# Kernel tuning notes

Hardware: AMD Instinct MI355X
Metric: run time of the kernel (lower is better)

The kernel has to match this reference:

```python
import jax, jax.numpy as jnp
import numpy as np

DIM = 256
NUM_HEADS = 8
WINDOW = 8


def setup_inputs() -> dict:
    key = jax.random.key(0)
    k1, k2, k3 = jax.random.split(key, 3)
    x = jax.random.normal(k1, (4, DIM, 256, 256), dtype=jnp.float32)
    w_qkv = jax.random.normal(k2, (3 * DIM, DIM), dtype=jnp.float32) * 0.02
    w_proj = jax.random.normal(k3, (DIM, DIM), dtype=jnp.float32) * 0.02
    return {"x": x, "w_qkv": w_qkv, "w_proj": w_proj}


def reference(x, w_qkv, w_proj):
    B, C, H, W = x.shape
    ws = WINDOW
    nh = NUM_HEADS
    hd = C // nh
    scale = float(hd) ** -0.5

    pad_h = (ws - H % ws) % ws
    pad_w = (ws - W % ws) % ws
    if pad_h or pad_w:
        x = jnp.pad(x, ((0, 0), (0, 0), (0, pad_h), (0, pad_w)))
    Hp, Wp = H + pad_h, W + pad_w
    nHw, nWw = Hp // ws, Wp // ws
    N = ws * ws

    # 1x1 conv QKV projection (no bias): [3C,C] x [B,C,Hp,Wp]
    qkv = jnp.einsum('oc,bchw->bohw', w_qkv, x)
    q, k, v = jnp.split(qkv, 3, axis=1)

    def partition(t):
        # [B,C,Hp,Wp] -> [B*nHw*nWw, nh, N, hd]
        t = t.reshape(B, nh, hd, nHw, ws, nWw, ws)
        t = t.transpose(0, 3, 5, 1, 4, 6, 2)  # B,nHw,nWw,nh,ws,ws,hd
        return t.reshape(B * nHw * nWw, nh, N, hd)

    qw = partition(q)
    kw = partition(k)
    vw = partition(v)

    attn = jnp.einsum('whnd,whmd->whnm', qw, kw) * scale
    attn = jax.nn.softmax(attn, axis=-1)
    out = jnp.einsum('whnm,whmd->whnd', attn, vw)  # [Bn, nh, N, hd]

    # unpartition: [Bn,nh,N,hd] -> [B,C,Hp,Wp]
    out = out.reshape(B, nHw, nWw, nh, ws, ws, hd)
    out = out.transpose(0, 3, 6, 1, 4, 2, 5)  # B,nh,hd,nHw,ws,nWw,ws
    out = out.reshape(B, C, Hp, Wp)

    out = jnp.einsum('oc,bchw->bohw', w_proj, out)
    if pad_h:
        out = out[:, :, :H, :]
    if pad_w:
        out = out[:, :, :, :W]
    return out
```

## Files before the change

kernel.cpp:

```cpp
#include <hip/hip_runtime.h>


#define DIMC 256
#define NH   8
#define HD   32
#define WS   8
#define NTOK 64
#define HRES 256
#define IMG  (HRES * HRES)

typedef _Float16 f16x8 __attribute__((ext_vector_type(8)));
typedef _Float16 f16x4 __attribute__((ext_vector_type(4)));
typedef float    f32x4 __attribute__((ext_vector_type(4)));

#define MFMA(a, b, c) __builtin_amdgcn_mfma_f32_16x16x32_f16((a), (b), (c), 0, 0, 0)

__global__ __launch_bounds__(256) void cvt_weights(const float* __restrict__ wqkv,
                                                   const float* __restrict__ wproj,
                                                   _Float16* __restrict__ wq,
                                                   _Float16* __restrict__ wp)
{
    int i = blockIdx.x * 256 + threadIdx.x;
    const int NQ = 768 * 256;
    const int NT = NQ + 256 * 256;
    if (i < NQ)      wq[i] = (_Float16)wqkv[i];
    else if (i < NT) wp[i - NQ] = (_Float16)wproj[i - NQ];
}

template <int PRE>
__device__ __forceinline__ f16x8 ldw(const void* w, int idx)
{
    if constexpr (PRE) {
        return *(const f16x8*)((const _Float16*)w + idx);
    } else {
        const float* p = (const float*)w + idx;
        f16x8 r;
        #pragma unroll
        for (int j = 0; j < 8; ++j) r[j] = (_Float16)p[j];
        return r;
    }
}

template <int PRE>
__global__ __launch_bounds__(512, 4)
void win_attn_mfma(const float* __restrict__ x,
                   const void* __restrict__ wqkv,
                   const void* __restrict__ wproj,
                   float* __restrict__ out)
{
    __shared__ _Float16 x_t[NTOK][DIMC + 8];
    __shared__ _Float16 q_t[NTOK][HD + 8];
    __shared__ _Float16 k_t[NTOK][HD + 8];
    __shared__ _Float16 v_c[HD][NTOK + 8];
    __shared__ _Float16 p_t[NTOK][NTOK + 8];
    __shared__ _Float16 ao_t[NTOK][HD + 8];

    const int t  = threadIdx.x;
    const int ln = t & 15;
    const int lq = (t & 63) >> 4;
    const int gu = __builtin_amdgcn_readfirstlane(t >> 6);
    const int b  = blockIdx.z;
    const int y0 = blockIdx.y * WS;
    const int x0 = blockIdx.x * WS;

    {
        const float* xb = x + (long)b * DIMC * IMG + (long)y0 * HRES + x0;
        #pragma unroll
        for (int i = 0; i < 4; ++i) {
            int qq = i * 512 + t;
            int c = qq >> 3, py = qq & 7;
            const float* src = xb + (long)c * IMG + py * HRES;
            float4 f0 = *(const float4*)src;
            float4 f1 = *(const float4*)(src + 4);
            int n = py * 8;
            x_t[n + 0][c] = (_Float16)f0.x; x_t[n + 1][c] = (_Float16)f0.y;
            x_t[n + 2][c] = (_Float16)f0.z; x_t[n + 3][c] = (_Float16)f0.w;
            x_t[n + 4][c] = (_Float16)f1.x; x_t[n + 5][c] = (_Float16)f1.y;
            x_t[n + 6][c] = (_Float16)f1.z; x_t[n + 7][c] = (_Float16)f1.w;
        }
    }

    const f32x4 zero = {0.f, 0.f, 0.f, 0.f};
    f32x4 facc[8];
    #pragma unroll
    for (int i = 0; i < 8; ++i) facc[i] = zero;

    const float scale = 0.17677669529663687f;
    const int nt = gu & 3;
    const int og = (gu >> 2) * 3;
    const int nrow = nt * 16 + ln;

    auto qkv_head = [&](int h) {
        f32x4 a0c = zero, a1c = zero, a2c = zero;
        const int wr0 = (((og + 0) >> 1) * DIMC + h * HD + (((og + 0) & 1) << 4) + ln) * DIMC;
        const int wr1 = (((og + 1) >> 1) * DIMC + h * HD + (((og + 1) & 1) << 4) + ln) * DIMC;
        const int wr2 = (((og + 2) >> 1) * DIMC + h * HD + (((og + 2) & 1) << 4) + ln) * DIMC;
        #pragma unroll
        for (int c0 = 0; c0 < DIMC; c0 += 32) {
            const int co = c0 + 8 * lq;
            f16x8 bx = *(const f16x8*)&x_t[nrow][co];
            f16x8 a0 = ldw<PRE>(wqkv, wr0 + co);
            f16x8 a1 = ldw<PRE>(wqkv, wr1 + co);
            f16x8 a2 = ldw<PRE>(wqkv, wr2 + co);
            a0c = MFMA(a0, bx, a0c);
            a1c = MFMA(a1, bx, a1c);
            a2c = MFMA(a2, bx, a2c);
        }
        #pragma unroll
        for (int j = 0; j < 3; ++j) {
            f32x4 a = (j == 0) ? a0c : ((j == 1) ? a1c : a2c);
            const int ot = og + j;
            const int part = ot >> 1;
            const int dbase = ((ot & 1) << 4) + 4 * lq;
            #pragma unroll
            for (int r = 0; r < 4; ++r) {
                const float v = a[r];
                const int d = dbase + r;
                if (part == 0)      q_t[nrow][d] = (_Float16)(v * scale);
                else if (part == 1) k_t[nrow][d] = (_Float16)v;
                else                v_c[d][nrow]  = (_Float16)v;
            }
        }
    };

    auto attn_head = [&]() {
        if (gu < 4) {
            const int qn = gu * 16 + ln;
            const int d8 = 8 * lq;
            f16x8 qf = *(const f16x8*)&q_t[qn][d8];
            f16x8 kf0 = *(const f16x8*)&k_t[ 0 + ln][d8];
            f16x8 kf1 = *(const f16x8*)&k_t[16 + ln][d8];
            f16x8 kf2 = *(const f16x8*)&k_t[32 + ln][d8];
            f16x8 kf3 = *(const f16x8*)&k_t[48 + ln][d8];
            f32x4 s0 = MFMA(kf0, qf, zero);
            f32x4 s1 = MFMA(kf1, qf, zero);
            f32x4 s2 = MFMA(kf2, qf, zero);
            f32x4 s3 = MFMA(kf3, qf, zero);
            float mx = -1e30f;
            #pragma unroll
            for (int r = 0; r < 4; ++r)
                mx = fmaxf(mx, fmaxf(fmaxf(s0[r], s1[r]), fmaxf(s2[r], s3[r])));
            mx = fmaxf(mx, __shfl_xor(mx, 16));
            mx = fmaxf(mx, __shfl_xor(mx, 32));
            float sum = 0.f;
            #pragma unroll
            for (int r = 0; r < 4; ++r) {
                s0[r] = __expf(s0[r] - mx); sum += s0[r];
                s1[r] = __expf(s1[r] - mx); sum += s1[r];
                s2[r] = __expf(s2[r] - mx); sum += s2[r];
                s3[r] = __expf(s3[r] - mx); sum += s3[r];
            }
            sum += __shfl_xor(sum, 16);
            sum += __shfl_xor(sum, 32);
            const float inv = 1.f / sum;
            const int kb = 4 * lq;
            f16x4 pv;
            #pragma unroll
            for (int r = 0; r < 4; ++r) pv[r] = (_Float16)(s0[r] * inv);
            *(f16x4*)&p_t[qn][ 0 + kb] = pv;
            #pragma unroll
            for (int r = 0; r < 4; ++r) pv[r] = (_Float16)(s1[r] * inv);
            *(f16x4*)&p_t[qn][16 + kb] = pv;
            #pragma unroll
            for (int r = 0; r < 4; ++r) pv[r] = (_Float16)(s2[r] * inv);
            *(f16x4*)&p_t[qn][32 + kb] = pv;
            #pragma unroll
            for (int r = 0; r < 4; ++r) pv[r] = (_Float16)(s3[r] * inv);
            *(f16x4*)&p_t[qn][48 + kb] = pv;

            f32x4 o0 = zero, o1 = zero;
            #pragma unroll
            for (int ks = 0; ks < 2; ++ks) {
                const int m0 = ks * 32 + 8 * lq;
                f16x8 pf = *(const f16x8*)&p_t[qn][m0];
                f16x8 v0 = *(const f16x8*)&v_c[ 0 + ln][m0];
                f16x8 v1 = *(const f16x8*)&v_c[16 + ln][m0];
                o0 = MFMA(v0, pf, o0);
                o1 = MFMA(v1, pf, o1);
            }
            const int db = 4 * lq;
            f16x4 av;
            #pragma unroll
            for (int r = 0; r < 4; ++r) av[r] = (_Float16)o0[r];
            *(f16x4*)&ao_t[qn][db] = av;
            #pragma unroll
            for (int r = 0; r < 4; ++r) av[r] = (_Float16)o1[r];
            *(f16x4*)&ao_t[qn][16 + db] = av;
        }
    };

    auto proj_head = [&](int h) {
        const int cb = h * HD + 8 * lq;
        f16x8 a0 = ldw<PRE>(wproj, ((gu * 2 + 0) * 16 + ln) * DIMC + cb);
        f16x8 a1 = ldw<PRE>(wproj, ((gu * 2 + 1) * 16 + ln) * DIMC + cb);
        #pragma unroll
        for (int np = 0; np < 4; ++np) {
            f16x8 bv = *(const f16x8*)&ao_t[np * 16 + ln][8 * lq];
            facc[np]     = MFMA(a0, bv, facc[np]);
            facc[4 + np] = MFMA(a1, bv, facc[4 + np]);
        }
    };

    __syncthreads();
    qkv_head(0);
    __syncthreads();
    for (int h = 0; h < NH; ++h) {
        attn_head();
        __syncthreads();
        proj_head(h);
        if (h < NH - 1) qkv_head(h + 1);
        __syncthreads();
    }

    {
        float* ob = out + (long)b * DIMC * IMG + (long)y0 * HRES + x0;
        #pragma unroll
        for (int i = 0; i < 8; ++i) {
            const int ot = gu * 2 + (i >> 2);
            const int n  = (i & 3) * 16 + ln;
            const int py = n >> 3, pxx = n & 7;
            float* op = ob + (long)(ot * 16 + 4 * lq) * IMG + py * HRES + pxx;
            op[0 * IMG] = facc[i][0];
            op[1 * IMG] = facc[i][1];
            op[2 * IMG] = facc[i][2];
            op[3 * IMG] = facc[i][3];
        }
    }
}

extern "C" void kernel_launch(void* const* d_in, const int* in_sizes, int n_in,
                              void* d_out, int out_size, void* d_ws, size_t ws_size,
                              hipStream_t stream)
{
    const float* x      = (const float*)d_in[0];
    const float* w_qkv  = (const float*)d_in[1];
    const float* w_proj = (const float*)d_in[2];
    float* out          = (float*)d_out;

    dim3 grid(HRES / WS, HRES / WS, 4);
    dim3 block(512);

    const size_t need = (size_t)(768 * 256 + 256 * 256) * sizeof(_Float16);
    if (d_ws && ws_size >= need) {
        _Float16* wq = (_Float16*)d_ws;
        _Float16* wp = wq + 768 * 256;
        hipLaunchKernelGGL(cvt_weights, dim3(1024), dim3(256), 0, stream,
                           w_qkv, w_proj, wq, wp);
        hipLaunchKernelGGL((win_attn_mfma<1>), grid, block, 0, stream,
                           x, (const void*)wq, (const void*)wp, out);
    } else {
        hipLaunchKernelGGL((win_attn_mfma<0>), grid, block, 0, stream,
                           x, (const void*)w_qkv, (const void*)w_proj, out);
    }
}
```

Measured before the change: 1.266 ms.

## Assign one head per wave and keep QKV/attention fragments in registers

The per-head loop with eight block-wide barriers is replaced by one head per wavefront. Q, K, V and P are kept in registers and rearranged into MFMA operand layout with lane shuffles instead of shared memory. The input tile is transposed with xor-shuffles so it can be written to shared memory as vectors, the full attention output is staged once before a single projection GEMM, and block indices are swizzled to change which windows run together. The cost is more registers and shuffle instructions per wave, which may lower occupancy.

```diff
diff --git a/kernel.cpp b/kernel.cpp
--- a/kernel.cpp
+++ b/kernel.cpp
@@ -9,6 +9,8 @@
 #define HRES 256
 #define IMG  (HRES * HRES)
 
+#define XPITCH 272
+
 typedef _Float16 f16x8 __attribute__((ext_vector_type(8)));
 typedef _Float16 f16x4 __attribute__((ext_vector_type(4)));
 typedef float    f32x4 __attribute__((ext_vector_type(4)));
@@ -39,6 +41,37 @@
         for (int j = 0; j < 8; ++j) r[j] = (_Float16)p[j];
         return r;
     }
+}
+
+__device__ __forceinline__ int2 shfl2(int2 v, int s)
+{
+    v.x = __shfl(v.x, s);
+    v.y = __shfl(v.y, s);
+    return v;
+}
+
+__device__ __forceinline__ int2 pack4(f32x4 a)
+{
+    f16x4 h;
+    h[0] = (_Float16)a[0]; h[1] = (_Float16)a[1];
+    h[2] = (_Float16)a[2]; h[3] = (_Float16)a[3];
+    return __builtin_bit_cast(int2, h);
+}
+
+__device__ __forceinline__ f16x8 cat8(int2 lo, int2 hi)
+{
+    int4 w = {lo.x, lo.y, hi.x, hi.y};
+    return __builtin_bit_cast(f16x8, w);
+}
+
+__device__ __forceinline__ f16x8 bfrag(int2 pu0, int2 pu1, int ln, int lq)
+{
+    const int slo = ln + 32 * (lq & 1);
+    int2 l0 = shfl2(pu0, slo), h0 = shfl2(pu0, slo + 16);
+    int2 l1 = shfl2(pu1, slo), h1 = shfl2(pu1, slo + 16);
+    int2 lo = (lq & 2) ? l1 : l0;
+    int2 hi = (lq & 2) ? h1 : h0;
+    return cat8(lo, hi);
 }
 
 template <int PRE>
@@ -48,183 +81,196 @@
                    const void* __restrict__ wproj,
                    float* __restrict__ out)
 {
-    __shared__ _Float16 x_t[NTOK][DIMC + 8];
-    __shared__ _Float16 q_t[NTOK][HD + 8];
-    __shared__ _Float16 k_t[NTOK][HD + 8];
-    __shared__ _Float16 v_c[HD][NTOK + 8];
-    __shared__ _Float16 p_t[NTOK][NTOK + 8];
-    __shared__ _Float16 ao_t[NTOK][HD + 8];
+    __shared__ _Float16 x_t[NTOK][XPITCH];
+    __shared__ _Float16 ao_t[NTOK][XPITCH];
 
     const int t  = threadIdx.x;
     const int ln = t & 15;
     const int lq = (t & 63) >> 4;
     const int gu = __builtin_amdgcn_readfirstlane(t >> 6);
-    const int b  = blockIdx.z;
-    const int y0 = blockIdx.y * WS;
-    const int x0 = blockIdx.x * WS;
+
+    const int lin = blockIdx.x + (blockIdx.y << 5) + (blockIdx.z << 10);
+    const int w   = ((lin & 7) << 9) | (lin >> 3);
+    const int b   = w >> 10;
+    const int y0  = ((w >> 5) & 31) * WS;
+    const int x0  = (w & 31) * WS;
+
+    const f32x4 zero = {0.f, 0.f, 0.f, 0.f};
+    const float scale = 0.17677669529663687f;
 
     {
-        const float* xb = x + (long)b * DIMC * IMG + (long)y0 * HRES + x0;
+        const int py = t & 7;
+        const int cg = (t & 63) >> 3;
+        const float* xb = x + (long)b * DIMC * IMG + (long)(y0 + py) * HRES + x0;
         #pragma unroll
         for (int i = 0; i < 4; ++i) {
-            int qq = i * 512 + t;
-            int c = qq >> 3, py = qq & 7;
-            const float* src = xb + (long)c * IMG + py * HRES;
+            const int cbase = i * 64 + gu * 8;
+            const float* src = xb + (long)(cbase + cg) * IMG;
             float4 f0 = *(const float4*)src;
             float4 f1 = *(const float4*)(src + 4);
-            int n = py * 8;
-            x_t[n + 0][c] = (_Float16)f0.x; x_t[n + 1][c] = (_Float16)f0.y;
-            x_t[n + 2][c] = (_Float16)f0.z; x_t[n + 3][c] = (_Float16)f0.w;
-            x_t[n + 4][c] = (_Float16)f1.x; x_t[n + 5][c] = (_Float16)f1.y;
-            x_t[n + 6][c] = (_Float16)f1.z; x_t[n + 7][c] = (_Float16)f1.w;
-        }
-    }
-
-    const f32x4 zero = {0.f, 0.f, 0.f, 0.f};
-    f32x4 facc[8];
+            float v[8] = {f0.x, f0.y, f0.z, f0.w, f1.x, f1.y, f1.z, f1.w};
+            #pragma unroll
+            for (int s = 1; s < 8; s <<= 1) {
+                float nv[8];
+                #pragma unroll
+                for (int j = 0; j < 8; ++j) {
+                    float ex = __shfl_xor(v[j ^ s], 8 * s);
+                    nv[j] = ((j ^ cg) & s) ? ex : v[j];
+                }
+                #pragma unroll
+                for (int j = 0; j < 8; ++j) v[j] = nv[j];
+            }
+            f16x8 hv;
+            #pragma unroll
+            for (int j = 0; j < 8; ++j) hv[j] = (_Float16)v[j];
+            *(f16x8*)&x_t[8 * py + cg][cbase] = hv;
+        }
+    }
+    __syncthreads();
+
+    int2 Qp[2][4], Kp[2][4], Vp[4][2];
     #pragma unroll
-    for (int i = 0; i < 8; ++i) facc[i] = zero;
-
-    const float scale = 0.17677669529663687f;
-    const int nt = gu & 3;
-    const int og = (gu >> 2) * 3;
-    const int nrow = nt * 16 + ln;
-
-    auto qkv_head = [&](int h) {
-        f32x4 a0c = zero, a1c = zero, a2c = zero;
-        const int wr0 = (((og + 0) >> 1) * DIMC + h * HD + (((og + 0) & 1) << 4) + ln) * DIMC;
-        const int wr1 = (((og + 1) >> 1) * DIMC + h * HD + (((og + 1) & 1) << 4) + ln) * DIMC;
-        const int wr2 = (((og + 2) >> 1) * DIMC + h * HD + (((og + 2) & 1) << 4) + ln) * DIMC;
-        #pragma unroll
-        for (int c0 = 0; c0 < DIMC; c0 += 32) {
-            const int co = c0 + 8 * lq;
-            f16x8 bx = *(const f16x8*)&x_t[nrow][co];
-            f16x8 a0 = ldw<PRE>(wqkv, wr0 + co);
-            f16x8 a1 = ldw<PRE>(wqkv, wr1 + co);
-            f16x8 a2 = ldw<PRE>(wqkv, wr2 + co);
-            a0c = MFMA(a0, bx, a0c);
-            a1c = MFMA(a1, bx, a1c);
-            a2c = MFMA(a2, bx, a2c);
-        }
-        #pragma unroll
-        for (int j = 0; j < 3; ++j) {
-            f32x4 a = (j == 0) ? a0c : ((j == 1) ? a1c : a2c);
-            const int ot = og + j;
-            const int part = ot >> 1;
-            const int dbase = ((ot & 1) << 4) + 4 * lq;
-            #pragma unroll
-            for (int r = 0; r < 4; ++r) {
-                const float v = a[r];
-                const int d = dbase + r;
-                if (part == 0)      q_t[nrow][d] = (_Float16)(v * scale);
-                else if (part == 1) k_t[nrow][d] = (_Float16)v;
-                else                v_c[d][nrow]  = (_Float16)v;
-            }
-        }
-    };
-
-    auto attn_head = [&]() {
-        if (gu < 4) {
-            const int qn = gu * 16 + ln;
-            const int d8 = 8 * lq;
-            f16x8 qf = *(const f16x8*)&q_t[qn][d8];
-            f16x8 kf0 = *(const f16x8*)&k_t[ 0 + ln][d8];
-            f16x8 kf1 = *(const f16x8*)&k_t[16 + ln][d8];
-            f16x8 kf2 = *(const f16x8*)&k_t[32 + ln][d8];
-            f16x8 kf3 = *(const f16x8*)&k_t[48 + ln][d8];
-            f32x4 s0 = MFMA(kf0, qf, zero);
-            f32x4 s1 = MFMA(kf1, qf, zero);
-            f32x4 s2 = MFMA(kf2, qf, zero);
-            f32x4 s3 = MFMA(kf3, qf, zero);
-            float mx = -1e30f;
-            #pragma unroll
-            for (int r = 0; r < 4; ++r)
-                mx = fmaxf(mx, fmaxf(fmaxf(s0[r], s1[r]), fmaxf(s2[r], s3[r])));
-            mx = fmaxf(mx, __shfl_xor(mx, 16));
-            mx = fmaxf(mx, __shfl_xor(mx, 32));
+    for (int mt = 0; mt < 2; ++mt) {
+        f32x4 aq[4], ak[4], av[4];
+        #pragma unroll
+        for (int nt = 0; nt < 4; ++nt) { aq[nt] = zero; ak[nt] = zero; av[nt] = zero; }
+        const int rq = (          gu * HD + 16 * mt + ln) * DIMC;
+        const int rk = (DIMC    + gu * HD + 16 * mt + ln) * DIMC;
+        const int rv = (2 * DIMC + gu * HD + 16 * mt + ln) * DIMC;
+        #pragma unroll
+        for (int ks = 0; ks < 8; ++ks) {
+            const int co = 32 * ks + 8 * lq;
+            f16x8 wqf = ldw<PRE>(wqkv, rq + co);
+            f16x8 wkf = ldw<PRE>(wqkv, rk + co);
+            f16x8 wvf = ldw<PRE>(wqkv, rv + co);
+            #pragma unroll
+            for (int nt = 0; nt < 4; ++nt) {
+                f16x8 xf = *(const f16x8*)&x_t[16 * nt + ln][co];
+                aq[nt] = MFMA(wqf, xf, aq[nt]);
+                ak[nt] = MFMA(wkf, xf, ak[nt]);
+                av[nt] = MFMA(xf, wvf, av[nt]);
+            }
+        }
+        #pragma unroll
+        for (int nt = 0; nt < 4; ++nt) {
+            Qp[mt][nt] = pack4(aq[nt] * scale);
+            Kp[mt][nt] = pack4(ak[nt]);
+            Vp[nt][mt] = pack4(av[nt]);
+        }
+    }
+
+    {
+        f16x8 kf[4], qf[4];
+        #pragma unroll
+        for (int kt = 0; kt < 4; ++kt) kf[kt] = bfrag(Kp[0][kt], Kp[1][kt], ln, lq);
+        #pragma unroll
+        for (int qt = 0; qt < 4; ++qt) qf[qt] = bfrag(Qp[0][qt], Qp[1][qt], ln, lq);
+
+        f32x4 s[4][4];
+        #pragma unroll
+        for (int kt = 0; kt < 4; ++kt)
+            #pragma unroll
+            for (int qt = 0; qt < 4; ++qt)
+                s[kt][qt] = MFMA(kf[kt], qf[qt], zero);
+
+        float inv[4];
+        #pragma unroll
+        for (int qt = 0; qt < 4; ++qt) {
+            float m = -1e30f;
+            #pragma unroll
+            for (int kt = 0; kt < 4; ++kt)
+                #pragma unroll
+                for (int r = 0; r < 4; ++r) m = fmaxf(m, s[kt][qt][r]);
+            m = fmaxf(m, __shfl_xor(m, 16));
+            m = fmaxf(m, __shfl_xor(m, 32));
             float sum = 0.f;
             #pragma unroll
-            for (int r = 0; r < 4; ++r) {
-                s0[r] = __expf(s0[r] - mx); sum += s0[r];
-                s1[r] = __expf(s1[r] - mx); sum += s1[r];
-                s2[r] = __expf(s2[r] - mx); sum += s2[r];
-                s3[r] = __expf(s3[r] - mx); sum += s3[r];
-            }
+            for (int kt = 0; kt < 4; ++kt)
+                #pragma unroll
+                for (int r = 0; r < 4; ++r) {
+                    float e = __expf(s[kt][qt][r] - m);
+                    s[kt][qt][r] = e;
+                    sum += e;
+                }
             sum += __shfl_xor(sum, 16);
             sum += __shfl_xor(sum, 32);
-            const float inv = 1.f / sum;
-            const int kb = 4 * lq;
-            f16x4 pv;
-            #pragma unroll
-            for (int r = 0; r < 4; ++r) pv[r] = (_Float16)(s0[r] * inv);
-            *(f16x4*)&p_t[qn][ 0 + kb] = pv;
-            #pragma unroll
-            for (int r = 0; r < 4; ++r) pv[r] = (_Float16)(s1[r] * inv);
-            *(f16x4*)&p_t[qn][16 + kb] = pv;
-            #pragma unroll
-            for (int r = 0; r < 4; ++r) pv[r] = (_Float16)(s2[r] * inv);
-            *(f16x4*)&p_t[qn][32 + kb] = pv;
-            #pragma unroll
-            for (int r = 0; r < 4; ++r) pv[r] = (_Float16)(s3[r] * inv);
-            *(f16x4*)&p_t[qn][48 + kb] = pv;
-
-            f32x4 o0 = zero, o1 = zero;
-            #pragma unroll
-            for (int ks = 0; ks < 2; ++ks) {
-                const int m0 = ks * 32 + 8 * lq;
-                f16x8 pf = *(const f16x8*)&p_t[qn][m0];
-                f16x8 v0 = *(const f16x8*)&v_c[ 0 + ln][m0];
-                f16x8 v1 = *(const f16x8*)&v_c[16 + ln][m0];
-                o0 = MFMA(v0, pf, o0);
-                o1 = MFMA(v1, pf, o1);
-            }
-            const int db = 4 * lq;
-            f16x4 av;
-            #pragma unroll
-            for (int r = 0; r < 4; ++r) av[r] = (_Float16)o0[r];
-            *(f16x4*)&ao_t[qn][db] = av;
-            #pragma unroll
-            for (int r = 0; r < 4; ++r) av[r] = (_Float16)o1[r];
-            *(f16x4*)&ao_t[qn][16 + db] = av;
-        }
-    };
-
-    auto proj_head = [&](int h) {
-        const int cb = h * HD + 8 * lq;
-        f16x8 a0 = ldw<PRE>(wproj, ((gu * 2 + 0) * 16 + ln) * DIMC + cb);
-        f16x8 a1 = ldw<PRE>(wproj, ((gu * 2 + 1) * 16 + ln) * DIMC + cb);
-        #pragma unroll
-        for (int np = 0; np < 4; ++np) {
-            f16x8 bv = *(const f16x8*)&ao_t[np * 16 + ln][8 * lq];
-            facc[np]     = MFMA(a0, bv, facc[np]);
-            facc[4 + np] = MFMA(a1, bv, facc[4 + np]);
-        }
-    };
-
+            inv[qt] = 1.f / sum;
+        }
+
+        int2 Pp[4][4];
+        #pragma unroll
+        for (int kt = 0; kt < 4; ++kt)
+            #pragma unroll
+            for (int qt = 0; qt < 4; ++qt)
+                Pp[kt][qt] = pack4(s[kt][qt] * inv[qt]);
+
+        f32x4 pv[2][4];
+        #pragma unroll
+        for (int dt = 0; dt < 2; ++dt)
+            #pragma unroll
+            for (int qt = 0; qt < 4; ++qt) pv[dt][qt] = zero;
+        #pragma unroll
+        for (int ks = 0; ks < 2; ++ks) {
+            f16x8 vf[2], pf[4];
+            #pragma unroll
+            for (int dt = 0; dt < 2; ++dt)
+                vf[dt] = bfrag(Vp[2 * ks][dt], Vp[2 * ks + 1][dt], ln, lq);
+            #pragma unroll
+            for (int qt = 0; qt < 4; ++qt)
+                pf[qt] = bfrag(Pp[2 * ks][qt], Pp[2 * ks + 1][qt], ln, lq);
+            #pragma unroll
+            for (int dt = 0; dt < 2; ++dt)
+                #pragma unroll
+                for (int qt = 0; qt < 4; ++qt)
+                    pv[dt][qt] = MFMA(vf[dt], pf[qt], pv[dt][qt]);
+        }
+
+        #pragma unroll
+        for (int dt = 0; dt < 2; ++dt)
+            #pragma unroll
+            for (int qt = 0; qt < 4; ++qt) {
+                f16x4 hv;
+                #pragma unroll
+                for (int r = 0; r < 4; ++r) hv[r] = (_Float16)pv[dt][qt][r];
+                *(f16x4*)&ao_t[16 * qt + ln][gu * HD + 16 * dt + 4 * lq] = hv;
+            }
+    }
     __syncthreads();
-    qkv_head(0);
-    __syncthreads();
-    for (int h = 0; h < NH; ++h) {
-        attn_head();
-        __syncthreads();
-        proj_head(h);
-        if (h < NH - 1) qkv_head(h + 1);
-        __syncthreads();
+
+    f32x4 fa[2][4];
+    #pragma unroll
+    for (int o = 0; o < 2; ++o)
+        #pragma unroll
+        for (int nt = 0; nt < 4; ++nt) fa[o][nt] = zero;
+    {
+        const int r0 = (16 * (2 * gu + 0) + ln) * DIMC;
+        const int r1 = (16 * (2 * gu + 1) + ln) * DIMC;
+        #pragma unroll
+        for (int ks = 0; ks < 8; ++ks) {
+            const int co = 32 * ks + 8 * lq;
+            f16x8 w0 = ldw<PRE>(wproj, r0 + co);
+            f16x8 w1 = ldw<PRE>(wproj, r1 + co);
+            #pragma unroll
+            for (int nt = 0; nt < 4; ++nt) {
+                f16x8 af = *(const f16x8*)&ao_t[16 * nt + ln][co];
+                fa[0][nt] = MFMA(w0, af, fa[0][nt]);
+                fa[1][nt] = MFMA(w1, af, fa[1][nt]);
+            }
+        }
     }
 
     {
         float* ob = out + (long)b * DIMC * IMG + (long)y0 * HRES + x0;
         #pragma unroll
-        for (int i = 0; i < 8; ++i) {
-            const int ot = gu * 2 + (i >> 2);
-            const int n  = (i & 3) * 16 + ln;
-            const int py = n >> 3, pxx = n & 7;
-            float* op = ob + (long)(ot * 16 + 4 * lq) * IMG + py * HRES + pxx;
-            op[0 * IMG] = facc[i][0];
-            op[1 * IMG] = facc[i][1];
-            op[2 * IMG] = facc[i][2];
-            op[3 * IMG] = facc[i][3];
-        }
+        for (int o = 0; o < 2; ++o)
+            #pragma unroll
+            for (int nt = 0; nt < 4; ++nt) {
+                const int och = 16 * (2 * gu + o) + 4 * lq;
+                const int tok = 16 * nt + ln;
+                float* op = ob + (long)och * IMG + (tok >> 3) * HRES + (tok & 7);
+                #pragma unroll
+                for (int r = 0; r < 4; ++r) op[(long)r * IMG] = fa[o][nt][r];
+            }
     }
 }
 
```

Result: faster. 1.013 ms (-20.0%).
